# Optimization experiments

Measured on AMD Instinct MI355X. Metric: run time of the kernel, lower is better.

The kernel has to match this reference:

```python
import jax, jax.numpy as jnp
import numpy as np

M, IN, OUT = 8192, 4096, 4096
BITWIDTH = 7


def psto_shift_int32(x, shift):
    """Pseudo-stochastic right-shift of int32 x by `shift` bits -> int8.
    Faithful to PstoShiftInt32: floor-divide, derive a pseudo random number
    from the low half of the remainder, compare against the high half."""
    pow_s = jnp.left_shift(jnp.int32(1), shift)
    rt = jnp.floor_divide(x, pow_s)
    prob = jnp.abs(x - rt * pow_s)
    half_pow = jnp.left_shift(jnp.int32(1), shift // 2)
    qp = jnp.floor_divide(prob, half_pow)
    prn = prob - qp * half_pow
    prn = jnp.where(shift % 2 == 1, prn * 2, prn)
    dec = jnp.where(qp <= prn, jnp.int32(0), jnp.int32(1)) * jnp.sign(x)
    return jnp.clip(rt + dec, -127, 127).astype(jnp.int8)


def range_bitwidth(x):
    # RangeEstimate: ceil(log2(max|x|)), 0 if all-zero (torch also goes via float)
    m = jnp.max(jnp.abs(x)).astype(jnp.float32)
    return jnp.where(m == 0, jnp.int32(0), jnp.ceil(jnp.log2(m)).astype(jnp.int32))


def act_calc(acc, exp_in):
    """Shift int32 accumulator back to int8 and track the block exponent."""
    bw = range_bitwidth(acc)
    shift = bw - BITWIDTH
    # shift>1 -> shift by `shift`; shift==1 -> shift by 2; else -> plain int8 cast
    eff = jnp.where(shift > 1, shift, jnp.where(shift == 1, jnp.int32(2), jnp.int32(0)))
    rounded = psto_shift_int32(acc, jnp.maximum(eff, 0))
    out = jnp.where(eff > 0, rounded, acc.astype(jnp.int8))  # int8 cast wraps, as in torch
    exp_out = (exp_in + eff).astype(jnp.int8)
    return out, exp_out


def setup_inputs() -> dict:
    key = jax.random.key(0)
    k1, k2 = jax.random.split(key)
    # int8-valued tensors kept in int32 containers for the matmul accumulate
    act_in = jax.random.randint(k1, (M, IN), -127, 128, dtype=jnp.int32)
    weight = jax.random.randint(k2, (OUT, IN), -127, 128, dtype=jnp.int32)
    return {"act_in": act_in, "exp_in": -6, "weight": weight, "weight_exp": -9}


def reference(act_in, exp_in, weight, weight_exp):
    # the roundoff4 padding in the original is a no-op)
    acc = jnp.matmul(act_in, weight.T)  # [M, OUT] int32
    act_out, exp_out = act_calc(acc, jnp.int32(exp_in) + jnp.int32(weight_exp))
    return act_out, exp_out
```

## Files before the change

### kernel.cpp

```cpp
#include <hip/hip_runtime.h>
#include <stdint.h>
#include <math.h>

#define M_DIM 8192
#define N_DIM 4096
#define K_DIM 4096
#define BITWIDTH 7

#define BM 256
#define BN 128
#define BK 128

using i32x4  = __attribute__((ext_vector_type(4)))  int;
using i32x16 = __attribute__((ext_vector_type(16))) int;

__global__ __launch_bounds__(256) void pack_both_kernel(
        const int* __restrict__ act, const int* __restrict__ wt,
        uint32_t* __restrict__ a8p, uint32_t* __restrict__ w8,
        int* __restrict__ maxabs) {
    if (blockIdx.x == 0 && threadIdx.x == 0) *maxabs = 0;

    if (blockIdx.x < 8192) {
        const int tid = blockIdx.x * 256 + threadIdx.x;
        const int L  = tid & 63;
        const int kb = (tid >> 6) & 127;
        const int mb = tid >> 13;
        const size_t src = (size_t)(mb * 32 + (L & 31)) * K_DIM
                         + kb * 32 + (L >> 5) * 16;
        const int4* s = (const int4*)(act + src);
        uint32_t w[4];
#pragma unroll
        for (int q = 0; q < 4; ++q) {
            int4 v = s[q];
            w[q] = (uint32_t)(v.x & 0xFF) | ((uint32_t)(v.y & 0xFF) << 8)
                 | ((uint32_t)(v.z & 0xFF) << 16) | ((uint32_t)(v.w & 0xFF) << 24);
        }
        ((uint4*)a8p)[tid] = make_uint4(w[0], w[1], w[2], w[3]);
    } else {
        const int i = (blockIdx.x - 8192) * 256 + threadIdx.x;
        int4 a = ((const int4*)wt)[2 * i];
        int4 b = ((const int4*)wt)[2 * i + 1];
        uint32_t p0 = (uint32_t)(a.x & 0xFF) | ((uint32_t)(a.y & 0xFF) << 8)
                    | ((uint32_t)(a.z & 0xFF) << 16) | ((uint32_t)(a.w & 0xFF) << 24);
        uint32_t p1 = (uint32_t)(b.x & 0xFF) | ((uint32_t)(b.y & 0xFF) << 8)
                    | ((uint32_t)(b.z & 0xFF) << 16) | ((uint32_t)(b.w & 0xFF) << 24);
        ((uint2*)w8)[i] = make_uint2(p0, p1);
    }
}

__device__ __forceinline__ void gload_lds16(const int8_t* g, int8_t* lds) {
    __builtin_amdgcn_global_load_lds(
        (__attribute__((address_space(1))) void*)g,
        (__attribute__((address_space(3))) void*)lds,
        16, 0, 0);
}

__global__ __launch_bounds__(256, 2) void gemm_i8(
        const int8_t* __restrict__ A8p, const int8_t* __restrict__ B8,
        int* __restrict__ C, int* __restrict__ maxabs) {
    __shared__ __align__(16) int8_t Bs[BN * BK];
    __shared__ int wmaxs[4];

    const int tid  = threadIdx.x;
    const int wave = tid >> 6;
    const int lane = tid & 63;
    const int fr   = lane & 31;
    const int hl   = lane >> 5;

    const int row0 = blockIdx.y * BM;
    const int col0 = blockIdx.x * BN;

    const int wm = (wave >> 1) * 128;
    const int wn = (wave & 1) * 64;

    i32x16 acc[4][2];
#pragma unroll
    for (int i = 0; i < 4; ++i)
#pragma unroll
        for (int j = 0; j < 2; ++j)
            acc[i][j] = (i32x16)(0);

    const int srowoff = lane >> 3;
    const int schk    = ((lane & 7) ^ srowoff) << 4;
    const int8_t* bg  = B8 + (size_t)(col0 + wave * 8 + srowoff) * K_DIM + schk;
    const int ldsoB   = wave * 1024;

    const int mbase = (row0 + wm) >> 5;
    const int8_t* aBase = A8p + (size_t)mbase * 128 * 1024 + (size_t)lane * 16;

    const int swz = fr & 7;
    int boff[4][2];
#pragma unroll
    for (int kk = 0; kk < 4; ++kk) {
        const int co = (((kk * 2 + hl) ^ swz) << 4);
#pragma unroll
        for (int j = 0; j < 2; ++j)
            boff[kk][j] = (wn + j * 32 + fr) * BK + co;
    }

    for (int t = 0; t < K_DIM / BK; ++t) {
        const int k0 = t * BK;
        __syncthreads();
#pragma unroll
        for (int g = 0; g < 4; ++g)
            gload_lds16(bg + k0 + (size_t)(32 * g) * K_DIM,
                        Bs + g * 4096 + ldsoB);

        i32x4 af[16];
#pragma unroll
        for (int i = 0; i < 4; ++i)
#pragma unroll
            for (int kk = 0; kk < 4; ++kk)
                af[i * 4 + kk] = *(const i32x4*)(aBase
                    + (size_t)(i * 128 + t * 4 + kk) * 1024);

        __syncthreads();

#pragma unroll
        for (int kk = 0; kk < 4; ++kk) {
            i32x4 bf[2];
#pragma unroll
            for (int j = 0; j < 2; ++j)
                bf[j] = *(const i32x4*)(Bs + boff[kk][j]);
#pragma unroll
            for (int i = 0; i < 4; ++i)
#pragma unroll
                for (int j = 0; j < 2; ++j)
                    acc[i][j] = __builtin_amdgcn_mfma_i32_32x32x32_i8(
                        af[i * 4 + kk], bf[j], acc[i][j], 0, 0, 0);
        }
    }

    int mymax = 0;
    const int ccol = fr;
    const int rbase = hl << 2;
#pragma unroll
    for (int i = 0; i < 4; ++i) {
#pragma unroll
        for (int j = 0; j < 2; ++j) {
            int* p = C + (size_t)(row0 + wm + i * 32) * N_DIM
                       + (col0 + wn + j * 32 + ccol);
#pragma unroll
            for (int r = 0; r < 16; ++r) {
                int row = (r & 3) + 8 * (r >> 2) + rbase;
                int v = acc[i][j][r];
                p[(size_t)row * N_DIM] = v;
                int a = v < 0 ? -v : v;
                mymax = a > mymax ? a : mymax;
            }
        }
    }

#pragma unroll
    for (int off = 32; off > 0; off >>= 1) {
        int o = __shfl_down(mymax, off, 64);
        mymax = o > mymax ? o : mymax;
    }
    if (lane == 0) wmaxs[wave] = mymax;
    __syncthreads();
    if (tid == 0) {
        int bmx = wmaxs[0];
        for (int w = 1; w < 4; ++w) bmx = wmaxs[w] > bmx ? wmaxs[w] : bmx;
        atomicMax(maxabs, bmx);
    }
}

__device__ __forceinline__ int psto(int x, int eff) {
    if (eff > 0) {
        int rt   = x >> eff;
        int prob = x & ((1 << eff) - 1);
        int h    = eff >> 1;
        int qp   = prob >> h;
        int prn  = (prob & ((1 << h) - 1)) << (eff & 1);
        int sgn  = (x > 0) - (x < 0);
        int r    = rt + ((qp <= prn) ? 0 : sgn);
        r = r < -127 ? -127 : r;
        r = r > 127 ? 127 : r;
        return r;
    }
    return (int)(int8_t)x;
}

__global__ __launch_bounds__(256) void finalize_kernel(int* __restrict__ C,
        const int* __restrict__ maxabs,
        const int* __restrict__ exp_in,
        const int* __restrict__ wexp) {
    const int m = *maxabs;
    int bw = 0;
    if (m != 0) bw = (int)ceilf(log2f((float)m));
    const int shift = bw - BITWIDTH;
    const int eff = (shift > 1) ? shift : ((shift == 1) ? 2 : 0);

    const size_t idx = ((size_t)blockIdx.x * blockDim.x + threadIdx.x) * 8;
    int4 v0 = *(const int4*)(C + idx);
    int4 v1 = *(const int4*)(C + idx + 4);
    int4 o0, o1;
    o0.x = psto(v0.x, eff); o0.y = psto(v0.y, eff);
    o0.z = psto(v0.z, eff); o0.w = psto(v0.w, eff);
    o1.x = psto(v1.x, eff); o1.y = psto(v1.y, eff);
    o1.z = psto(v1.z, eff); o1.w = psto(v1.w, eff);
    *(int4*)(C + idx) = o0;
    *(int4*)(C + idx + 4) = o1;

    if (idx == 0) {
        C[(size_t)M_DIM * N_DIM] = (int)(int8_t)(exp_in[0] + wexp[0] + eff);
    }
}

extern "C" void kernel_launch(void* const* d_in, const int* in_sizes, int n_in,
                              void* d_out, int out_size, void* d_ws, size_t ws_size,
                              hipStream_t stream) {
    const int* act    = (const int*)d_in[0];
    const int* exp_in = (const int*)d_in[1];
    const int* wt     = (const int*)d_in[2];
    const int* wexp   = (const int*)d_in[3];

    int8_t* a8p    = (int8_t*)d_ws;
    int8_t* w8     = a8p + (size_t)M_DIM * K_DIM;
    int*    maxabs = (int*)(w8 + (size_t)N_DIM * K_DIM);

    pack_both_kernel<<<16384, 256, 0, stream>>>(
        act, wt, (uint32_t*)a8p, (uint32_t*)w8, maxabs);

    int* C = (int*)d_out;
    dim3 grid(N_DIM / BN, M_DIM / BM);
    gemm_i8<<<grid, 256, 0, stream>>>(a8p, w8, C, maxabs);

    finalize_kernel<<<((size_t)M_DIM * N_DIM / 8) / 256, 256, 0, stream>>>(
        C, maxabs, exp_in, wexp);
}
```

Measured before the change: 451.1 us.

## Double-buffer B tile in LDS and software-pipeline A fragment loads

```diff
diff --git a/kernel.cpp b/kernel.cpp
--- a/kernel.cpp
+++ b/kernel.cpp
@@ -10,9 +10,12 @@
 #define BM 256
 #define BN 128
 #define BK 128
+#define NT (K_DIM / BK)
 
 using i32x4  = __attribute__((ext_vector_type(4)))  int;
 using i32x16 = __attribute__((ext_vector_type(16))) int;
+
+#define FENCE asm volatile("" ::: "memory")
 
 __global__ __launch_bounds__(256) void pack_both_kernel(
         const int* __restrict__ act, const int* __restrict__ wt,
@@ -55,11 +58,30 @@
         16, 0, 0);
 }
 
+__device__ __forceinline__ void load_af(i32x4 (&d)[4], const int8_t* aBase,
+                                        int tkk) {
+#pragma unroll
+    for (int i = 0; i < 4; ++i)
+        d[i] = *(const i32x4*)(aBase + (size_t)((i * 128 + tkk) << 10));
+}
+
+__device__ __forceinline__ void kkstep(const i32x4 (&a)[4], const int8_t* bbuf,
+                                       const int (&bo)[2], i32x16 (&acc)[4][2]) {
+    i32x4 b0 = *(const i32x4*)(bbuf + bo[0]);
+    i32x4 b1 = *(const i32x4*)(bbuf + bo[1]);
+#pragma unroll
+    for (int i = 0; i < 4; ++i) {
+        acc[i][0] = __builtin_amdgcn_mfma_i32_32x32x32_i8(a[i], b0, acc[i][0], 0, 0, 0);
+        acc[i][1] = __builtin_amdgcn_mfma_i32_32x32x32_i8(a[i], b1, acc[i][1], 0, 0, 0);
+    }
+}
+
 __global__ __launch_bounds__(256, 2) void gemm_i8(
         const int8_t* __restrict__ A8p, const int8_t* __restrict__ B8,
         int* __restrict__ C, int* __restrict__ maxabs) {
-    __shared__ __align__(16) int8_t Bs[BN * BK];
+    __shared__ __align__(16) int8_t Bs[2][BN * BK];
     __shared__ int wmaxs[4];
+    int8_t* BsF = &Bs[0][0];
 
     const int tid  = threadIdx.x;
     const int wave = tid >> 6;
@@ -98,37 +120,46 @@
             boff[kk][j] = (wn + j * 32 + fr) * BK + co;
     }
 
-    for (int t = 0; t < K_DIM / BK; ++t) {
-        const int k0 = t * BK;
-        __syncthreads();
+    i32x4 afE[4], afO[4];
+
+#pragma unroll
+    for (int g = 0; g < 4; ++g)
+        gload_lds16(bg + (size_t)(32 * g) * K_DIM, BsF + ldsoB + g * 4096);
+    FENCE;
+    load_af(afE, aBase, 0);
+    asm volatile("s_waitcnt vmcnt(4)" ::: "memory");
+    __builtin_amdgcn_s_barrier();
+
+    for (int t = 0; t < NT - 1; ++t) {
+        const int8_t* bbuf = BsF + ((t & 1) << 14);
+        int8_t* bstg = BsF + (((t + 1) & 1) << 14) + ldsoB;
+        const int kg = (t + 1) * BK;
 #pragma unroll
         for (int g = 0; g < 4; ++g)
-            gload_lds16(bg + k0 + (size_t)(32 * g) * K_DIM,
-                        Bs + g * 4096 + ldsoB);
-
-        i32x4 af[16];
-#pragma unroll
-        for (int i = 0; i < 4; ++i)
-#pragma unroll
-            for (int kk = 0; kk < 4; ++kk)
-                af[i * 4 + kk] = *(const i32x4*)(aBase
-                    + (size_t)(i * 128 + t * 4 + kk) * 1024);
-
-        __syncthreads();
-
-#pragma unroll
-        for (int kk = 0; kk < 4; ++kk) {
-            i32x4 bf[2];
-#pragma unroll
-            for (int j = 0; j < 2; ++j)
-                bf[j] = *(const i32x4*)(Bs + boff[kk][j]);
-#pragma unroll
-            for (int i = 0; i < 4; ++i)
-#pragma unroll
-                for (int j = 0; j < 2; ++j)
-                    acc[i][j] = __builtin_amdgcn_mfma_i32_32x32x32_i8(
-                        af[i * 4 + kk], bf[j], acc[i][j], 0, 0, 0);
-        }
+            gload_lds16(bg + kg + (size_t)(32 * g) * K_DIM, bstg + g * 4096);
+        FENCE;
+        load_af(afO, aBase, t * 4 + 1); FENCE;
+        kkstep(afE, bbuf, boff[0], acc);
+        load_af(afE, aBase, t * 4 + 2); FENCE;
+        kkstep(afO, bbuf, boff[1], acc);
+        load_af(afO, aBase, t * 4 + 3); FENCE;
+        kkstep(afE, bbuf, boff[2], acc);
+        load_af(afE, aBase, t * 4 + 4); FENCE;
+        kkstep(afO, bbuf, boff[3], acc);
+        asm volatile("s_waitcnt vmcnt(4)" ::: "memory");
+        __builtin_amdgcn_s_barrier();
+    }
+
+    {
+        const int tl = NT - 1;
+        const int8_t* bbuf = BsF + ((tl & 1) << 14);
+        load_af(afO, aBase, tl * 4 + 1);
+        kkstep(afE, bbuf, boff[0], acc);
+        load_af(afE, aBase, tl * 4 + 2);
+        kkstep(afO, bbuf, boff[1], acc);
+        load_af(afO, aBase, tl * 4 + 3);
+        kkstep(afE, bbuf, boff[2], acc);
+        kkstep(afO, bbuf, boff[3], acc);
     }
 
     int mymax = 0;
```

Measured after the change: 440.1 us. 2.4% less time.
